# Optimization experiments

Hardware: AMD Instinct MI355X
Metric: run time of the kernel (lower is better)

Reference implementation:

```python
import jax, jax.numpy as jnp
import numpy as np

B, K = 2048, 128
M = 5 * K
ALPHA = 1.0 / K          # alpha_k = 1/K
VARTHETA = 0.1
PMAX = 10.0
BIG = 1e9


def _gnn(HW, X, W0a, W1a, W0b, W1b):
    """Order-1 graph filter GNN (HWGCN, K0=[1,1]): relu hidden layer, linear output.
    HW: (B,K,K), X: (B,K,Fin) -> (B,K,Fout)."""
    SX = jnp.einsum('bij,bjf->bif', HW, X)
    Z = jax.nn.relu(X @ W0a + SX @ W1a)              # (B,K,32)
    SZ = jnp.einsum('bij,bjh->bih', HW, Z)
    return Z @ W0b + SZ @ W1b                        # (B,K,Fout)


def setup_inputs() -> dict:
    key = jax.random.key(0)
    ks = jax.random.split(key, 16)
    s = 0.05
    d = {
        'num_itr': 10,
        'kth': 9,
        'HW': jnp.abs(jax.random.normal(ks[0], (B, K, K), jnp.float32)) * s,
        'x0_tmp': jax.random.uniform(ks[1], (B, M), jnp.float32),
        'nu3_val': jnp.array([0.1], jnp.float32),
        'tilde_gamma_val': jnp.array([2.0], jnp.float32),
        'A9': jax.random.normal(ks[2], (1,), jnp.float32),
        'A1': jax.random.normal(ks[3], (1,), jnp.float32),
        'A3': jax.random.normal(ks[4], (1,), jnp.float32),
        'A7': jax.random.normal(ks[5], (1,), jnp.float32),
        'b7': jax.random.normal(ks[6], (1,), jnp.float32),
        'A10': jax.random.normal(ks[7], (1,), jnp.float32),
        'g1_W0a': jax.random.normal(ks[8], (5, 32), jnp.float32) * s,
        'g1_W1a': jax.random.normal(ks[9], (5, 32), jnp.float32) * s,
        'g1_W0b': jax.random.normal(ks[10], (32, 2), jnp.float32) * s,
        'g1_W1b': jax.random.normal(ks[11], (32, 2), jnp.float32) * s,
        'g2_W0a': jax.random.normal(ks[12], (K + 5, 32), jnp.float32) * s,
        'g2_W1a': jax.random.normal(ks[13], (K + 5, 32), jnp.float32) * s,
        'g2_W0b': jax.random.normal(ks[14], (32, 5), jnp.float32) * s,
        'g2_W1b': jax.random.normal(ks[15], (32, 5), jnp.float32) * s,
    }
    return d


def reference(num_itr, kth, HW, x0_tmp, nu3_val, tilde_gamma_val,
              A9, A1, A3, A7, b7, A10,
              g1_W0a, g1_W1a, g1_W0b, g1_W1b,
              g2_W0a, g2_W1a, g2_W0b, g2_W1b):
    nu3 = nu3_val[0]
    tg = tilde_gamma_val[0]
    x = x0_tmp                                        # (B, 5K)

    # REGNN 1 -> step sizes lbd (B,2)
    X1 = x.reshape(B, 5, K).transpose(0, 2, 1)        # (B,K,5)
    lbd = jax.nn.relu(jnp.mean(_gnn(HW, X1, g1_W0a, g1_W1a, g1_W0b, g1_W1b), axis=1))

    # vectorized per-K gradient steps on segments [K:2K] and [4K:5K]
    s0, s1, s2, s3, s4 = (x[:, i * K:(i + 1) * K] for i in range(5))
    s1 = s1 - lbd[:, 0:1] * (ALPHA / (1.0 + s1))
    s4 = s4 + lbd[:, 1:2] * (ALPHA * VARTHETA)
    x = jnp.concatenate([s0, s1, s2, s3, s4], axis=1)

    # REGNN 2 correction
    X2 = x.reshape(B, 5, K).transpose(0, 2, 1)        # (B,K,5)
    tilde = _gnn(HW, jnp.concatenate([HW, X2], axis=-1),
                 g2_W0a, g2_W1a, g2_W0b, g2_W1b)      # (B,K,5)
    x = x + tilde.transpose(0, 2, 1).reshape(B, M)

    # proj onto C8: sum of first K entries <= Pmax (||q||^2 = K)
    f = jnp.sum(x[:, :K], axis=1) - PMAX              # (B,)
    q = jnp.concatenate([jnp.ones(K, x.dtype), jnp.zeros(4 * K, x.dtype)])
    x = jnp.where((f <= 0)[:, None], x, x - f[:, None] * q / K)

    # banded elementwise box clamps (faithful sequential max/min)
    idx = jnp.arange(M)
    band = lambda a, b: (idx >= a) & (idx < b)
    Vnu = 1.0 - 1.0 / (1.0 + nu3) ** 2
    Vg = 1.0 - 1.0 / (1.0 + tg) ** 2
    x = jnp.maximum(jnp.where(band(K, 2 * K), nu3, 0.0), x)
    x = jnp.minimum(jnp.where(band(2 * K, 3 * K), tg, BIG), x)
    x = jnp.maximum(jnp.where(band(3 * K, 4 * K), Vnu, 0.0), x)
    x = jnp.minimum(jnp.where(band(3 * K, 4 * K), Vg, BIG), x)

    if kth == num_itr - 1:  # static python branch
        x = jnp.maximum(x, 0.0)
        xg = x[:, 2 * K:3 * K]   # gamma
        xv = x[:, 3 * K:4 * K]   # V
        f5 = 1.0 - 1.0 / (1.0 + xg) ** 2 - xv
        f6 = jnp.sqrt(xv) - x[:, 4 * K:5 * K]
        p = x[:, 0:K]
        nu = x[:, K:2 * K]
        diagHW = jnp.diagonal(HW, axis1=1, axis2=2)   # (B,K)
        top = p * diagHW
        down = jnp.einsum('bi,bij->bj', p, HW) - top + 1.0
        f4 = top - down * xg
        f2 = nu * down - top
        return (x, f5, f6, f4, f2)
    return (x,)
```

## Files before the change

kernel.cpp:

```cpp
#include <hip/hip_runtime.h>
#include <math.h>

#define B_N 2048
#define KK 128
#define MM 640
#define HS 136
#define ZSS 40
#define SXS 12
#define ALPHA (1.0f/128.0f)
#define VARTHETA 0.1f
#define PMAXV 10.0f
#define BIGV 1000000000.0f

typedef __attribute__((ext_vector_type(8))) short short8;
typedef __attribute__((ext_vector_type(4))) short short4v;
typedef __attribute__((ext_vector_type(4))) float floatx4;
typedef __attribute__((ext_vector_type(4))) __bf16 bf16x4;

static __device__ __forceinline__ unsigned short f2bf(float f) {
    return __builtin_bit_cast(unsigned short, (__bf16)f);
}
static __device__ __forceinline__ short4v cvt4(floatx4 v) {
    return __builtin_bit_cast(short4v, __builtin_convertvector(v, bf16x4));
}
static __device__ __forceinline__ float bf2f(unsigned short h) {
    unsigned u = ((unsigned)h) << 16;
    return __builtin_bit_cast(float, u);
}

#define POOLA_OFF 0
#define POOLB_OFF 10240
#define POOL_BYTES (10240 + 8704)

__global__ __launch_bounds__(512, 4)
void unfold_pocs_kernel(
    const int* __restrict__ num_itr_p, const int* __restrict__ kth_p,
    const float* __restrict__ HW, const float* __restrict__ x0,
    const float* __restrict__ nu3_p, const float* __restrict__ tg_p,
    const float* __restrict__ g1_W0a, const float* __restrict__ g1_W1a,
    const float* __restrict__ g1_W0b, const float* __restrict__ g1_W1b,
    const float* __restrict__ g2_W0a, const float* __restrict__ g2_W1a,
    const float* __restrict__ g2_W0b, const float* __restrict__ g2_W1b,
    float* __restrict__ out)
{
    __shared__ __align__(16) unsigned short hwb[KK*HS];
    __shared__ __align__(16) unsigned char pool[POOL_BYTES];
    __shared__ __align__(16) float xb[MM];
    __shared__ __align__(16) unsigned short xbf[5*HS];
    __shared__ __align__(16) unsigned short x2bf[KK*8];
    __shared__ __align__(16) unsigned short w1abf[32*8];
    __shared__ __align__(16) unsigned short w0abf[32*8];
    __shared__ __align__(16) float g1w0a[160], g1w1a[160];
    __shared__ __align__(16) float g1w0b[64],  g1w1b[64];
    __shared__ __align__(16) float w0b2[160],  w1b2[160];
    __shared__ float red[16];

    unsigned short* w1aT = (unsigned short*)(pool + POOLA_OFF);
    unsigned short* zbp  = (unsigned short*)(pool + POOLA_OFF);
    float*          SXs  = (float*)(pool + POOLB_OFF);
    unsigned short* c2T  = (unsigned short*)(pool + POOLB_OFF);
    unsigned short* eT   = (unsigned short*)(pool + POOLB_OFF);
    float*          t0f  = (float*)(pool + POOLB_OFF + 2048);

    const int t = threadIdx.x;
    const int b = blockIdx.x;
    const float* HWb = HW + (size_t)b * (KK*KK);

    const int wv = t >> 6, lane = t & 63, quad = lane >> 4, lr = lane & 15;
    const int arow = wv*16 + lr;

    #pragma unroll
    for (int it = 0; it < 8; ++it) {
        int qi = it * 512 + t;
        int row = qi >> 5, q = qi & 31;
        floatx4 v = *(const floatx4*)(HWb + row*KK + q*4);
        *(short4v*)&hwb[row*HS + q*4] = cvt4(v);
    }
    {
        const int n = t & 31, seg = t >> 5;
        unsigned short tmp[8];
        #pragma unroll
        for (int i = 0; i < 8; ++i) tmp[i] = f2bf(g2_W1a[(seg*8 + i)*32 + n]);
        *(short8*)&w1aT[n*HS + seg*8] = *(short8*)tmp;
    }
    {
        const int n = (t & 255) >> 3, j = t & 7;
        if (t < 256) w1abf[t]       = (j < 5) ? f2bf(g2_W1a[(KK + j)*32 + n]) : (unsigned short)0;
        else if (t < 512) w0abf[t - 256] = (j < 5) ? f2bf(g2_W0a[(KK + j)*32 + n]) : (unsigned short)0;
    }
    if (t < 160) {
        floatx4 v = *(const floatx4*)(x0 + (size_t)b*MM + t*4);
        *(floatx4*)(xb + t*4) = v;
        *(short4v*)&xbf[(t >> 5)*HS + ((t*4) & 127)] = cvt4(v);
        g1w0a[t] = g1_W0a[t];
        g1w1a[t] = g1_W1a[t];
        w0b2[t]  = g2_W0b[t];
        w1b2[t]  = g2_W1b[t];
    }
    if (t < 64) { g1w0b[t] = g1_W0b[t]; g1w1b[t] = g1_W1b[t]; }
    __syncthreads();

    {
        floatx4 acc = {0.f, 0.f, 0.f, 0.f};
        const int ns = lr < 5 ? lr : 4;
        #pragma unroll
        for (int kt = 0; kt < 4; ++kt) {
            short8 a  = *(const short8*)&hwb[arow*HS + kt*32 + quad*8];
            short8 bb = *(const short8*)&xbf[ns*HS   + kt*32 + quad*8];
            acc = __builtin_amdgcn_mfma_f32_16x16x32_bf16(a, bb, acc, 0, 0, 0);
        }
        if (lr < 5) {
            #pragma unroll
            for (int r = 0; r < 4; ++r)
                SXs[(wv*16 + quad*4 + r)*SXS + lr] = acc[r];
        }
    }
    __syncthreads();

    const int row = t >> 2, g = t & 3;

    {
        float sx[5], x1r[5];
        #pragma unroll
        for (int f = 0; f < 5; ++f) { sx[f] = SXs[row*SXS + f]; x1r[f] = xb[f*KK + row]; }

        float zb0p0=0, zb0p1=0, zb1p0=0, zb1p1=0;
        #pragma unroll
        for (int hh = 0; hh < 8; ++hh) {
            int h = 8*g + hh;
            float a = 0.0f;
            #pragma unroll
            for (int f = 0; f < 5; ++f) a += x1r[f]*g1w0a[f*32+h] + sx[f]*g1w1a[f*32+h];
            a = fmaxf(a, 0.0f);
            zb0p0 += a * g1w0b[h*2+0];
            zb0p1 += a * g1w0b[h*2+1];
            zb1p0 += a * g1w1b[h*2+0];
            zb1p1 += a * g1w1b[h*2+1];
        }
        float mp = 0.0f;
        for (int w = 0; w < 32; ++w) {
            int i = 4*w + g;
            mp += bf2f(hwb[i*HS + row]);
        }
        mp += __shfl_xor(mp, 1); mp += __shfl_xor(mp, 2);
        float m = mp * (1.0f/KK);
        float c0 = zb0p0*(1.0f/KK) + m*zb1p0;
        float c1 = zb0p1*(1.0f/KK) + m*zb1p1;
        #pragma unroll
        for (int s = 1; s < 64; s <<= 1) { c0 += __shfl_xor(c0, s); c1 += __shfl_xor(c1, s); }
        if (lane == 0) { red[wv*2] = c0; red[wv*2 + 1] = c1; }
    }
    __syncthreads();

    {
        float lbd0 = 0.f, lbd1 = 0.f;
        #pragma unroll
        for (int w2 = 0; w2 < 8; ++w2) { lbd0 += red[w2*2]; lbd1 += red[w2*2+1]; }
        lbd0 = fmaxf(lbd0, 0.0f); lbd1 = fmaxf(lbd1, 0.0f);

        const int i0 = 2*t, m = i0 >> 3, f0 = i0 & 7;
        float va = (f0     < 5) ? xb[f0*KK + m]     : 0.f;
        float vb = (f0 + 1 < 5) ? xb[(f0+1)*KK + m] : 0.f;
        if (f0 == 0) { vb = vb - lbd0 * (ALPHA / (1.0f + vb)); xb[KK + m]   = vb; }
        if (f0 == 4) { va = va + lbd1 * (ALPHA * VARTHETA);    xb[4*KK + m] = va; }
        ushort2 p; p.x = f2bf(va); p.y = f2bf(vb);
        *(ushort2*)&x2bf[i0] = p;
    }
    __syncthreads();

    short8 A[4];
    #pragma unroll
    for (int kt = 0; kt < 4; ++kt)
        A[kt] = *(const short8*)&hwb[arow*HS + kt*32 + quad*8];

    #pragma unroll
    for (int nt = 0; nt < 2; ++nt) {
        const int n = nt*16 + lr, mmb = wv*16 + quad*4;
        floatx4 acc = {0.f, 0.f, 0.f, 0.f};
        short8 ax2 = {0,0,0,0,0,0,0,0}, bx2 = {0,0,0,0,0,0,0,0};
        if (quad == 0) {
            ax2 = *(const short8*)&x2bf[(wv*16 + lr)*8];
            bx2 = *(const short8*)&w1abf[n*8];
        }
        acc = __builtin_amdgcn_mfma_f32_16x16x32_bf16(ax2, bx2, acc, 0, 0, 0);
        #pragma unroll
        for (int kt = 0; kt < 4; ++kt) {
            short8 bb = *(const short8*)&w1aT[n*HS + kt*32 + quad*8];
            acc = __builtin_amdgcn_mfma_f32_16x16x32_bf16(A[kt], bb, acc, 0, 0, 0);
        }
        ushort4 pe;
        pe.x = f2bf(acc[0] + g2_W0a[(mmb+0)*32 + n]);
        pe.y = f2bf(acc[1] + g2_W0a[(mmb+1)*32 + n]);
        pe.z = f2bf(acc[2] + g2_W0a[(mmb+2)*32 + n]);
        pe.w = f2bf(acc[3] + g2_W0a[(mmb+3)*32 + n]);
        *(ushort4*)&c2T[n*HS + mmb] = pe;
    }
    __syncthreads();

    #pragma unroll
    for (int nt = 0; nt < 2; ++nt) {
        const int n = nt*16 + lr, mmb = wv*16 + quad*4;
        floatx4 acc = {0.f, 0.f, 0.f, 0.f};
        short8 ax2 = {0,0,0,0,0,0,0,0}, bx2 = {0,0,0,0,0,0,0,0};
        if (quad == 0) {
            ax2 = *(const short8*)&x2bf[(wv*16 + lr)*8];
            bx2 = *(const short8*)&w0abf[n*8];
        }
        acc = __builtin_amdgcn_mfma_f32_16x16x32_bf16(ax2, bx2, acc, 0, 0, 0);
        #pragma unroll
        for (int kt = 0; kt < 4; ++kt) {
            short8 bb = *(const short8*)&c2T[n*HS + kt*32 + quad*8];
            acc = __builtin_amdgcn_mfma_f32_16x16x32_bf16(A[kt], bb, acc, 0, 0, 0);
        }
        #pragma unroll
        for (int r = 0; r < 4; ++r)
            zbp[(mmb + r)*ZSS + n] = f2bf(fmaxf(acc[r], 0.0f));
    }
    __syncthreads();

    {
        float ev[5] = {0,0,0,0,0}, t0v[5] = {0,0,0,0,0};
        short8 zrow = *(const short8*)&zbp[row*ZSS + g*8];
        #pragma unroll
        for (int hh = 0; hh < 8; ++hh) {
            int h = 8*g + hh;
            float zv = bf2f((unsigned short)zrow[hh]);
            #pragma unroll
            for (int c = 0; c < 5; ++c) {
                ev[c]  += zv * w1b2[h*5 + c];
                t0v[c] += zv * w0b2[h*5 + c];
            }
        }
        #pragma unroll
        for (int c = 0; c < 5; ++c) {
            ev[c]  += __shfl_xor(ev[c], 1);  ev[c]  += __shfl_xor(ev[c], 2);
            t0v[c] += __shfl_xor(t0v[c], 1); t0v[c] += __shfl_xor(t0v[c], 2);
        }
        if (g == 0) {
            #pragma unroll
            for (int c = 0; c < 5; ++c) {
                eT[c*HS + row]  = f2bf(ev[c]);
                t0f[row*8 + c]  = t0v[c];
            }
        }
    }
    __syncthreads();

    {
        floatx4 acc = {0.f, 0.f, 0.f, 0.f};
        const int ns = lr < 5 ? lr : 4;
        #pragma unroll
        for (int kt = 0; kt < 4; ++kt) {
            short8 bb = *(const short8*)&eT[ns*HS + kt*32 + quad*8];
            acc = __builtin_amdgcn_mfma_f32_16x16x32_bf16(A[kt], bb, acc, 0, 0, 0);
        }
        if (lr < 5) {
            #pragma unroll
            for (int r = 0; r < 4; ++r) {
                int mm = wv*16 + quad*4 + r;
                xb[lr*KK + mm] += acc[r] + t0f[mm*8 + lr];
            }
        }
    }
    __syncthreads();

    float pv = (t < KK) ? xb[t] : 0.0f;
    #pragma unroll
    for (int s = 1; s < 64; s <<= 1) pv += __shfl_xor(pv, s);
    if (lane == 0) red[wv] = pv;
    __syncthreads();
    float fv = -PMAXV;
    #pragma unroll
    for (int w2 = 0; w2 < 8; ++w2) fv += red[w2];

    const int num_itr = num_itr_p[0], kth = kth_p[0];
    const bool flag = (kth == num_itr - 1);
    const float nu3 = nu3_p[0], tg = tg_p[0];
    const float onu = 1.0f + nu3, otg = 1.0f + tg;
    const float Vnu = 1.0f - 1.0f/(onu*onu), Vg = 1.0f - 1.0f/(otg*otg);
    float* outx = out + (size_t)b * MM;

    #pragma unroll
    for (int r2 = 0; r2 < 2; ++r2) {
        int idx = r2*512 + t;
        if (idx < MM) {
            float v = xb[idx];
            if (idx < KK && fv > 0.0f) v -= fv * (1.0f/KK);
            v = fmaxf(v, (idx >= KK   && idx < 2*KK) ? nu3 : 0.0f);
            v = fminf(v, (idx >= 2*KK && idx < 3*KK) ? tg  : BIGV);
            v = fmaxf(v, (idx >= 3*KK && idx < 4*KK) ? Vnu : 0.0f);
            v = fminf(v, (idx >= 3*KK && idx < 4*KK) ? Vg  : BIGV);
            if (flag) v = fmaxf(v, 0.0f);
            xb[idx] = v;
            outx[idx] = v;
        }
    }

    if (flag) {
        __syncthreads();
        const size_t O1 = (size_t)B_N*MM;
        const size_t OK = (size_t)B_N*KK;
        if (t < KK) {
            float xg = xb[2*KK + t], xv = xb[3*KK + t];
            float u1 = 1.0f + xg;
            out[O1 + (size_t)b*KK + t]      = 1.0f - 1.0f/(u1*u1) - xv;
            out[O1 + OK + (size_t)b*KK + t] = sqrtf(xv) - xb[4*KK + t];
        }
        float dp = 0.0f;
        for (int w = 0; w < 32; ++w) {
            int i = 4*w + g;
            dp += xb[i] * bf2f(hwb[i*HS + row]);
        }
        dp += __shfl_xor(dp, 1); dp += __shfl_xor(dp, 2);
        if (g == 0) {
            float p_  = xb[row], nuv = xb[KK + row], xg = xb[2*KK + row];
            float diag = bf2f(hwb[row*HS + row]);
            float top  = p_ * diag;
            float down = dp - top + 1.0f;
            out[O1 + 2*OK + (size_t)b*KK + row] = top - down * xg;
            out[O1 + 3*OK + (size_t)b*KK + row] = nuv * down - top;
        }
    }
}

extern "C" void kernel_launch(void* const* d_in, const int* in_sizes, int n_in,
                              void* d_out, int out_size, void* d_ws, size_t ws_size,
                              hipStream_t stream) {
    unfold_pocs_kernel<<<dim3(B_N), dim3(512), 0, stream>>>(
        (const int*)d_in[0], (const int*)d_in[1],
        (const float*)d_in[2], (const float*)d_in[3],
        (const float*)d_in[4], (const float*)d_in[5],
        (const float*)d_in[12], (const float*)d_in[13],
        (const float*)d_in[14], (const float*)d_in[15],
        (const float*)d_in[16], (const float*)d_in[17],
        (const float*)d_in[18], (const float*)d_in[19],
        (float*)d_out);
}
```

Measured before the change: 253.0 us.

## Keep HW tile in MFMA registers instead of LDS, compute column sums via shuffles

Removes the 34 KB bf16 copy of HW from shared memory. Each lane now loads its MFMA A-fragment directly from global memory and keeps it in registers for every use. Column sums (the mean for GNN1) and the p·HW products (for f4/f2) are computed with cross-lane shuffle reductions into a small per-wave buffer, and the diagonal is re-read from global memory. The launch bound is raised to 8 blocks per CU to use the freed LDS for more blocks, at the cost of many shuffles and more register pressure.

New measurement: 352.1 us. +39.1%, slower.

```diff
diff --git a/kernel.cpp b/kernel.cpp
--- a/kernel.cpp
+++ b/kernel.cpp
@@ -27,12 +27,16 @@
     unsigned u = ((unsigned)h) << 16;
     return __builtin_bit_cast(float, u);
 }
+static __device__ __forceinline__ short8 pack8(floatx4 lo, floatx4 hi) {
+    short4v a = cvt4(lo), b4 = cvt4(hi);
+    return __builtin_shufflevector(a, b4, 0, 1, 2, 3, 4, 5, 6, 7);
+}
 
 #define POOLA_OFF 0
 #define POOLB_OFF 10240
 #define POOL_BYTES (10240 + 8704)
 
-__global__ __launch_bounds__(512, 4)
+__global__ __launch_bounds__(512, 8)
 void unfold_pocs_kernel(
     const int* __restrict__ num_itr_p, const int* __restrict__ kth_p,
     const float* __restrict__ HW, const float* __restrict__ x0,
@@ -43,7 +47,6 @@
     const float* __restrict__ g2_W0b, const float* __restrict__ g2_W1b,
     float* __restrict__ out)
 {
-    __shared__ __align__(16) unsigned short hwb[KK*HS];
     __shared__ __align__(16) unsigned char pool[POOL_BYTES];
     __shared__ __align__(16) float xb[MM];
     __shared__ __align__(16) unsigned short xbf[5*HS];
@@ -53,6 +56,7 @@
     __shared__ __align__(16) float g1w0a[160], g1w1a[160];
     __shared__ __align__(16) float g1w0b[64],  g1w1b[64];
     __shared__ __align__(16) float w0b2[160],  w1b2[160];
+    __shared__ __align__(16) float cw[8*KK];
     __shared__ float red[16];
 
     unsigned short* w1aT = (unsigned short*)(pool + POOLA_OFF);
@@ -69,13 +73,23 @@
     const int wv = t >> 6, lane = t & 63, quad = lane >> 4, lr = lane & 15;
     const int arow = wv*16 + lr;
 
-    #pragma unroll
-    for (int it = 0; it < 8; ++it) {
-        int qi = it * 512 + t;
-        int row = qi >> 5, q = qi & 31;
-        floatx4 v = *(const floatx4*)(HWb + row*KK + q*4);
-        *(short4v*)&hwb[row*HS + q*4] = cvt4(v);
-    }
+    short8 A[4];
+    {
+        const float* arp = HWb + arow*KK + quad*8;
+        floatx4 t0 = *(const floatx4*)(arp);
+        floatx4 t1 = *(const floatx4*)(arp + 4);
+        floatx4 t2 = *(const floatx4*)(arp + 32);
+        floatx4 t3 = *(const floatx4*)(arp + 36);
+        A[0] = pack8(t0, t1);
+        A[1] = pack8(t2, t3);
+        t0 = *(const floatx4*)(arp + 64);
+        t1 = *(const floatx4*)(arp + 68);
+        t2 = *(const floatx4*)(arp + 96);
+        t3 = *(const floatx4*)(arp + 100);
+        A[2] = pack8(t0, t1);
+        A[3] = pack8(t2, t3);
+    }
+
     {
         const int n = t & 31, seg = t >> 5;
         unsigned short tmp[8];
@@ -98,6 +112,22 @@
         w1b2[t]  = g2_W1b[t];
     }
     if (t < 64) { g1w0b[t] = g1_W0b[t]; g1w1b[t] = g1_W1b[t]; }
+
+    #pragma unroll
+    for (int kt = 0; kt < 4; ++kt) {
+        float v[8];
+        #pragma unroll
+        for (int j = 0; j < 8; ++j) v[j] = bf2f((unsigned short)A[kt][j]);
+        #pragma unroll
+        for (int s = 1; s < 16; s <<= 1) {
+            #pragma unroll
+            for (int j = 0; j < 8; ++j) v[j] += __shfl_xor(v[j], s);
+        }
+        if (lr == 0) {
+            #pragma unroll
+            for (int j = 0; j < 8; ++j) cw[wv*KK + kt*32 + quad*8 + j] = v[j];
+        }
+    }
     __syncthreads();
 
     {
@@ -105,9 +135,8 @@
         const int ns = lr < 5 ? lr : 4;
         #pragma unroll
         for (int kt = 0; kt < 4; ++kt) {
-            short8 a  = *(const short8*)&hwb[arow*HS + kt*32 + quad*8];
-            short8 bb = *(const short8*)&xbf[ns*HS   + kt*32 + quad*8];
-            acc = __builtin_amdgcn_mfma_f32_16x16x32_bf16(a, bb, acc, 0, 0, 0);
+            short8 bb = *(const short8*)&xbf[ns*HS + kt*32 + quad*8];
+            acc = __builtin_amdgcn_mfma_f32_16x16x32_bf16(A[kt], bb, acc, 0, 0, 0);
         }
         if (lr < 5) {
             #pragma unroll
@@ -138,11 +167,8 @@
             zb1p1 += a * g1w1b[h*2+1];
         }
         float mp = 0.0f;
-        for (int w = 0; w < 32; ++w) {
-            int i = 4*w + g;
-            mp += bf2f(hwb[i*HS + row]);
-        }
-        mp += __shfl_xor(mp, 1); mp += __shfl_xor(mp, 2);
+        #pragma unroll
+        for (int w = 0; w < 8; ++w) mp += cw[w*KK + row];
         float m = mp * (1.0f/KK);
         float c0 = zb0p0*(1.0f/KK) + m*zb1p0;
         float c1 = zb0p1*(1.0f/KK) + m*zb1p1;
@@ -167,11 +193,6 @@
         *(ushort2*)&x2bf[i0] = p;
     }
     __syncthreads();
-
-    short8 A[4];
-    #pragma unroll
-    for (int kt = 0; kt < 4; ++kt)
-        A[kt] = *(const short8*)&hwb[arow*HS + kt*32 + quad*8];
 
     #pragma unroll
     for (int nt = 0; nt < 2; ++nt) {
@@ -306,19 +327,35 @@
             out[O1 + (size_t)b*KK + t]      = 1.0f - 1.0f/(u1*u1) - xv;
             out[O1 + OK + (size_t)b*KK + t] = sqrtf(xv) - xb[4*KK + t];
         }
-        float dp = 0.0f;
-        for (int w = 0; w < 32; ++w) {
-            int i = 4*w + g;
-            dp += xb[i] * bf2f(hwb[i*HS + row]);
-        }
-        dp += __shfl_xor(dp, 1); dp += __shfl_xor(dp, 2);
-        if (g == 0) {
-            float p_  = xb[row], nuv = xb[KK + row], xg = xb[2*KK + row];
-            float diag = bf2f(hwb[row*HS + row]);
+        {
+            float pval = xb[arow];
+            #pragma unroll
+            for (int kt = 0; kt < 4; ++kt) {
+                float v[8];
+                #pragma unroll
+                for (int j = 0; j < 8; ++j) v[j] = pval * bf2f((unsigned short)A[kt][j]);
+                #pragma unroll
+                for (int s = 1; s < 16; s <<= 1) {
+                    #pragma unroll
+                    for (int j = 0; j < 8; ++j) v[j] += __shfl_xor(v[j], s);
+                }
+                if (lr == 0) {
+                    #pragma unroll
+                    for (int j = 0; j < 8; ++j) cw[wv*KK + kt*32 + quad*8 + j] = v[j];
+                }
+            }
+        }
+        __syncthreads();
+        if (t < KK) {
+            float dp = 0.0f;
+            #pragma unroll
+            for (int w = 0; w < 8; ++w) dp += cw[w*KK + t];
+            float p_  = xb[t], nuv = xb[KK + t], xg = xb[2*KK + t];
+            float diag = bf2f(f2bf(HWb[t*KK + t]));
             float top  = p_ * diag;
             float down = dp - top + 1.0f;
-            out[O1 + 2*OK + (size_t)b*KK + row] = top - down * xg;
-            out[O1 + 3*OK + (size_t)b*KK + row] = nuv * down - top;
+            out[O1 + 2*OK + (size_t)b*KK + t] = top - down * xg;
+            out[O1 + 3*OK + (size_t)b*KK + t] = nuv * down - top;
         }
     }
 }
```
